# Kernel tuning notes

Hardware: AMD Instinct MI355X
Metric: run time of the kernel (lower is better)

The kernel has to match this reference:

```python
import jax, jax.numpy as jnp
import numpy as np

H = 128  # hidden_size

def _band_agg(h):
    # Equivalent to bmm(adj, h) with adj = degree-normalized tridiagonal
    # (self + left + right neighbor), degree=3 interior, 2 at endpoints,
    # normalization adj/(deg+1e-8) as in the torch module.
    B, S, D = h.shape
    hp = jnp.pad(h, ((0, 0), (1, 1), (0, 0)))
    s = hp[:, :-2] + hp[:, 1:-1] + hp[:, 2:]            # [B,S,D] neighbor sum
    deg = jnp.full((S,), 3.0, dtype=h.dtype).at[0].set(2.0).at[S - 1].set(2.0)
    return s / (deg + 1e-8)[None, :, None]


def setup_inputs() -> dict:
    key = jax.random.key(0)
    ks = jax.random.split(key, 16)
    f32 = jnp.float32
    p = lambda k, shp: (jax.random.normal(k, shp, dtype=f32) * 0.05)
    return {
        "x": jax.random.normal(ks[0], (32, 2048, 6), dtype=f32),
        "enc_w1": p(ks[1], (6, H)),   "enc_b1": p(ks[2], (H,)),
        "enc_w2": p(ks[3], (H, H)),   "enc_b2": p(ks[4], (H,)),
        "gc1_w": p(ks[5], (H, H)),    "gc1_b": p(ks[6], (H,)),
        "gc2_w": p(ks[7], (H, H)),    "gc2_b": p(ks[8], (H,)),
        "gc3_w": p(ks[9], (H, H)),    "gc3_b": p(ks[10], (H,)),
        "cls_w1": p(ks[11], (H, H // 2)), "cls_b1": p(ks[12], (H // 2,)),
        "cls_w2": p(ks[13], (H // 2, 3)), "cls_b2": p(ks[14], (3,)),
    }


def reference(x, enc_w1, enc_b1, enc_w2, enc_b2,
              gc1_w, gc1_b, gc2_w, gc2_b, gc3_w, gc3_b,
              cls_w1, cls_b1, cls_w2, cls_b2):
    # node encoder: Linear -> ReLU -> Linear
    h = jax.nn.relu(x @ enc_w1 + enc_b1) @ enc_w2 + enc_b2
    # three graph convolutions: linear, normalized tridiagonal aggregate, relu
    h = jax.nn.relu(_band_agg(h @ gc1_w + gc1_b))
    h = jax.nn.relu(_band_agg(h @ gc2_w + gc2_b))
    h = jax.nn.relu(_band_agg(h @ gc3_w + gc3_b))
    # AdaptiveAvgPool1d(1) over seq dim after transpose == mean over nodes
    pooled = h.mean(axis=1)                              # [B, H]
    # classifier (dropout inactive in eval)
    return jax.nn.relu(pooled @ cls_w1 + cls_b1) @ cls_w2 + cls_b2
```

## Files before the change

kernel.cpp:

```cpp
#include <hip/hip_runtime.h>

#define SEQ  2048
#define HID  128
#define NB   32
#define TILE 58
#define GX   36
#define MSTR 67

typedef float f2    __attribute__((ext_vector_type(2)));
typedef float f32x4 __attribute__((ext_vector_type(4)));
typedef short bf16x8 __attribute__((ext_vector_type(8)));

__device__ __forceinline__ void split_bf16(float v, short& h, short& l) {
  unsigned u = __float_as_uint(v);
  unsigned r = (u + 0x7fffu + ((u >> 16) & 1u)) >> 16;
  h = (short)r;
  const float hf = __uint_as_float(r << 16);
  const float lo = v - hf;
  unsigned u2 = __float_as_uint(lo);
  unsigned r2 = (u2 + 0x7fffu + ((u2 >> 16) & 1u)) >> 16;
  l = (short)r2;
}

__global__ __launch_bounds__(256) void prep_fold(
    const float* __restrict__ enc_w2, const float* __restrict__ enc_b2,
    const float* __restrict__ gc1_w, const float* __restrict__ gc1_b,
    float* __restrict__ Wp, float* __restrict__ bp)
{
  const int tid = threadIdx.x;
  if (blockIdx.x < 16) {
    const int r = blockIdx.x * 8 + (tid >> 5);
    const int c = (tid & 31) * 4;
    float4 a = make_float4(0.f, 0.f, 0.f, 0.f);
    for (int k = 0; k < 128; ++k) {
      const float w = enc_w2[r * 128 + k];
      const float4 g = *(const float4*)&gc1_w[k * 128 + c];
      a.x = fmaf(w, g.x, a.x); a.y = fmaf(w, g.y, a.y);
      a.z = fmaf(w, g.z, a.z); a.w = fmaf(w, g.w, a.w);
    }
    *(float4*)&Wp[r * 128 + c] = a;
  } else if (tid < 128) {
    float s = gc1_b[tid];
    for (int k = 0; k < 128; ++k) s = fmaf(enc_b2[k], gc1_w[k * 128 + tid], s);
    bp[tid] = s;
  }
}

__global__ __launch_bounds__(256) void prep_shuffle(
    const float* __restrict__ Wp, const float* __restrict__ gc2_w,
    const float* __restrict__ gc3_w, short* __restrict__ Wf)
{
  const int L = blockIdx.y;
  const float* SW = (L == 0) ? Wp : (L == 1) ? gc2_w : gc3_w;
  const int ks = blockIdx.x >> 3, nt = blockIdx.x & 7;
  short* hi = Wf + L * 32768;
  short* lo = hi + 16384;
  for (int f = threadIdx.x; f < 512; f += 256) {
    const int l = f >> 3, j = f & 7;
    const int k = ks * 32 + (l >> 4) * 8 + j;
    const int n = nt * 16 + (l & 15);
    short h, lw;
    split_bf16(SW[k * 128 + n], h, lw);
    const int d = ((ks * 8 + nt) * 64 + l) * 8 + j;
    hi[d] = h; lo[d] = lw;
  }
}

__global__ __launch_bounds__(256) void fused_kernel(
    const float* __restrict__ x,
    const float* __restrict__ enc_w1, const float* __restrict__ enc_b1,
    const short* __restrict__ Wf, const float* __restrict__ bp,
    const float* __restrict__ gc2_b, const float* __restrict__ gc3_b,
    float* __restrict__ partial)
{
  __shared__ float hT[HID * MSTR];
  __shared__ float wsmall[7 * HID];
  __shared__ float psum[256];

  const int tid  = threadIdx.x;
  const int lane = tid & 63;
  const int w    = tid >> 6;
  const int gxb  = blockIdx.x, b = blockIdx.y;
  const int s0   = gxb * TILE;

  for (int f = tid; f < 7 * HID; f += 256)
    wsmall[f] = (f < 6 * HID) ? enc_w1[f] : enc_b1[f - 6 * HID];

  const int sm = s0 - 3 + lane;
  float xv[6];
  if (sm >= 0 && sm < SEQ) {
    const f2* xp = (const f2*)(x + ((long long)b * SEQ + sm) * 6);
    const f2 a0 = xp[0], a1 = xp[1], a2 = xp[2];
    xv[0] = a0.x; xv[1] = a0.y; xv[2] = a1.x;
    xv[3] = a1.y; xv[4] = a2.x; xv[5] = a2.y;
  } else {
    #pragma unroll
    for (int k = 0; k < 6; ++k) xv[k] = 0.f;
  }
  __syncthreads();
  {
    const int c0 = w * 32;
    float4 a4[8];
    #pragma unroll
    for (int q = 0; q < 8; ++q) a4[q] = make_float4(0.f, 0.f, 0.f, 0.f);
    #pragma unroll
    for (int k = 0; k < 6; ++k) {
      #pragma unroll
      for (int q = 0; q < 8; ++q) {
        const float4 wv = *(const float4*)&wsmall[k * HID + c0 + q * 4];
        a4[q].x = fmaf(xv[k], wv.x, a4[q].x);
        a4[q].y = fmaf(xv[k], wv.y, a4[q].y);
        a4[q].z = fmaf(xv[k], wv.z, a4[q].z);
        a4[q].w = fmaf(xv[k], wv.w, a4[q].w);
      }
    }
    #pragma unroll
    for (int q = 0; q < 8; ++q) {
      const float4 bb = *(const float4*)&wsmall[6 * HID + c0 + q * 4];
      const int c = c0 + q * 4;
      hT[(c + 0) * MSTR + lane] = fmaxf(a4[q].x + bb.x, 0.f);
      hT[(c + 1) * MSTR + lane] = fmaxf(a4[q].y + bb.y, 0.f);
      hT[(c + 2) * MSTR + lane] = fmaxf(a4[q].z + bb.z, 0.f);
      hT[(c + 3) * MSTR + lane] = fmaxf(a4[q].w + bb.w, 0.f);
    }
  }
  __syncthreads();

  const int mt   = w * 16 + (lane & 15);
  const int koct = (lane >> 4) * 8;
  const int stt  = s0 - 3 + mt;
  const float invdA = (stt == 0 || stt == SEQ - 1) ? (1.0f / (2.0f + 1e-8f))
                                                   : (1.0f / (3.0f + 1e-8f));
  const int mm = (mt == 0) ? 0 : mt - 1;
  const int mp = (mt == 63) ? 63 : mt + 1;

  #pragma unroll 1
  for (int L = 0; L < 3; ++L) {
    const short* WfL = Wf + L * 32768;
    const bf16x8* Bhi = (const bf16x8*)WfL;
    const bf16x8* Blo = (const bf16x8*)(WfL + 16384);
    const float* bias = (L == 0) ? bp : (L == 1) ? gc2_b : gc3_b;

    f32x4 acc[8];
    #pragma unroll
    for (int nt = 0; nt < 8; ++nt) acc[nt] = (f32x4){0.f, 0.f, 0.f, 0.f};

    #pragma unroll 1
    for (int ks = 0; ks < 4; ++ks) {
      const int fb = ks * 512 + lane;
      bf16x8 bh[8], bl[8];
      #pragma unroll
      for (int nt = 0; nt < 8; ++nt) {
        bh[nt] = Bhi[fb + nt * 64];
        bl[nt] = Blo[fb + nt * 64];
      }
      bf16x8 ah, al;
      const float* pa = &hT[(ks * 32 + koct) * MSTR];
      #pragma unroll
      for (int j = 0; j < 8; ++j) {
        float v;
        if (L == 0) {
          v = pa[j * MSTR + mt];
        } else {
          v = (pa[j * MSTR + mm] + pa[j * MSTR + mt] + pa[j * MSTR + mp]) * invdA;
          v = fmaxf(v, 0.f);
        }
        short h, lo;
        split_bf16(v, h, lo);
        ah[j] = h; al[j] = lo;
      }
      #pragma unroll
      for (int nt = 0; nt < 8; ++nt) {
        acc[nt] = __builtin_amdgcn_mfma_f32_16x16x32_bf16(ah, bh[nt], acc[nt], 0, 0, 0);
        acc[nt] = __builtin_amdgcn_mfma_f32_16x16x32_bf16(ah, bl[nt], acc[nt], 0, 0, 0);
        acc[nt] = __builtin_amdgcn_mfma_f32_16x16x32_bf16(al, bh[nt], acc[nt], 0, 0, 0);
      }
    }
    __syncthreads();

    {
      const int n0 = lane & 15;
      const int mrow0 = w * 16 + (lane >> 4) * 4;
      #pragma unroll
      for (int nt = 0; nt < 8; ++nt) {
        const float bn = bias[nt * 16 + n0];
        float* pw = &hT[(nt * 16 + n0) * MSTR];
        #pragma unroll
        for (int r = 0; r < 4; ++r) {
          const int m = mrow0 + r;
          const int s = s0 - 3 + m;
          const bool vld = (s >= 0 && s < SEQ);
          pw[m] = vld ? (acc[nt][r] + bn) : 0.f;
        }
      }
    }
    __syncthreads();
  }

  {
    const int c = tid & 127, half = tid >> 7;
    float ps = 0.f;
    const float* pc = &hT[c * MSTR];
    #pragma unroll 1
    for (int r = 0; r < 29; ++r) {
      const int m = 3 + half * 29 + r;
      const int s = s0 + half * 29 + r;
      if (s < SEQ) {
        const float invd = (s == 0 || s == SEQ - 1) ? (1.0f / (2.0f + 1e-8f))
                                                    : (1.0f / (3.0f + 1e-8f));
        ps += fmaxf((pc[m - 1] + pc[m] + pc[m + 1]) * invd, 0.f);
      }
    }
    psum[tid] = ps;
  }
  __syncthreads();
  if (tid < 128)
    partial[((long long)b * GX + gxb) * HID + tid] = psum[tid] + psum[tid + 128];
}

__global__ __launch_bounds__(128) void cls_kernel(
    const float* __restrict__ partial,
    const float* __restrict__ w1, const float* __restrict__ b1,
    const float* __restrict__ w2, const float* __restrict__ b2,
    float* __restrict__ out)
{
  __shared__ float ms[128];
  __shared__ float hid[64];
  const int b = blockIdx.x, tid = threadIdx.x;
  float a = 0.f;
  #pragma unroll 1
  for (int g = 0; g < GX; ++g) a += partial[((long long)b * GX + g) * HID + tid];
  ms[tid] = a * (1.0f / 2048.0f);
  __syncthreads();
  if (tid < 64) {
    float h = b1[tid];
    for (int k = 0; k < 128; ++k) h = fmaf(ms[k], w1[k * 64 + tid], h);
    hid[tid] = fmaxf(h, 0.f);
  }
  __syncthreads();
  if (tid < 3) {
    float o = b2[tid];
    for (int k = 0; k < 64; ++k) o = fmaf(hid[k], w2[k * 3 + tid], o);
    out[b * 3 + tid] = o;
  }
}

extern "C" void kernel_launch(void* const* d_in, const int* in_sizes, int n_in,
                              void* d_out, int out_size, void* d_ws, size_t ws_size,
                              hipStream_t stream) {
  (void)in_sizes; (void)n_in; (void)out_size; (void)ws_size;
  const float* x      = (const float*)d_in[0];
  const float* enc_w1 = (const float*)d_in[1];
  const float* enc_b1 = (const float*)d_in[2];
  const float* enc_w2 = (const float*)d_in[3];
  const float* enc_b2 = (const float*)d_in[4];
  const float* gc1_w  = (const float*)d_in[5];
  const float* gc1_b  = (const float*)d_in[6];
  const float* gc2_w  = (const float*)d_in[7];
  const float* gc2_b  = (const float*)d_in[8];
  const float* gc3_w  = (const float*)d_in[9];
  const float* gc3_b  = (const float*)d_in[10];
  const float* cls_w1 = (const float*)d_in[11];
  const float* cls_b1 = (const float*)d_in[12];
  const float* cls_w2 = (const float*)d_in[13];
  const float* cls_b2 = (const float*)d_in[14];

  float* Wp      = (float*)d_ws;
  float* bpv     = Wp + 16384;
  short* Wfrag   = (short*)(bpv + 128);
  float* partial = (float*)(Wfrag + 3 * 2 * 16384);

  prep_fold<<<dim3(17), 256, 0, stream>>>(enc_w2, enc_b2, gc1_w, gc1_b, Wp, bpv);
  prep_shuffle<<<dim3(32, 3), 256, 0, stream>>>(Wp, gc2_w, gc3_w, Wfrag);
  fused_kernel<<<dim3(GX, NB), 256, 0, stream>>>(
      x, enc_w1, enc_b1, Wfrag, bpv, gc2_b, gc3_b, partial);
  cls_kernel<<<dim3(NB), 128, 0, stream>>>(partial, cls_w1, cls_b1, cls_w2, cls_b2,
                                           (float*)d_out);
}
```

Before: 147.4 us.

## Merge weight-fold and bf16 shuffle prep into one kernel; parallelize classifier

The two preprocessing kernels (folding enc_w2 into gc1_w, then splitting and shuffling all three weight matrices into bf16 hi/lo fragments) become a single kernel launch. Each block stages a 32-row k-slice in shared memory before splitting it. This drops one launch and the fp32 Wp round trip through global memory. The classifier kernel now runs 256 threads and splits the partial-sum reduction and the first linear layer across thread groups to shorten the serial loops. The cost is a small 12-block prep grid, which leaves fold parallelism low.

```diff
diff --git a/kernel.cpp b/kernel.cpp
--- a/kernel.cpp
+++ b/kernel.cpp
@@ -22,47 +22,67 @@
   l = (short)r2;
 }
 
-__global__ __launch_bounds__(256) void prep_fold(
+__global__ __launch_bounds__(256) void prep_kernel(
     const float* __restrict__ enc_w2, const float* __restrict__ enc_b2,
     const float* __restrict__ gc1_w, const float* __restrict__ gc1_b,
-    float* __restrict__ Wp, float* __restrict__ bp)
+    const float* __restrict__ gc2_w, const float* __restrict__ gc3_w,
+    short* __restrict__ Wf, float* __restrict__ bp)
 {
+  __shared__ float Wls[32][130];
+  __shared__ float ew2s[32][128];
+  __shared__ float bsum[2][128];
+
+  const int ks = blockIdx.x;
+  const int L  = blockIdx.y;
   const int tid = threadIdx.x;
-  if (blockIdx.x < 16) {
-    const int r = blockIdx.x * 8 + (tid >> 5);
-    const int c = (tid & 31) * 4;
-    float4 a = make_float4(0.f, 0.f, 0.f, 0.f);
-    for (int k = 0; k < 128; ++k) {
-      const float w = enc_w2[r * 128 + k];
-      const float4 g = *(const float4*)&gc1_w[k * 128 + c];
-      a.x = fmaf(w, g.x, a.x); a.y = fmaf(w, g.y, a.y);
-      a.z = fmaf(w, g.z, a.z); a.w = fmaf(w, g.w, a.w);
-    }
-    *(float4*)&Wp[r * 128 + c] = a;
-  } else if (tid < 128) {
-    float s = gc1_b[tid];
-    for (int k = 0; k < 128; ++k) s = fmaf(enc_b2[k], gc1_w[k * 128 + tid], s);
-    bp[tid] = s;
-  }
-}
-
-__global__ __launch_bounds__(256) void prep_shuffle(
-    const float* __restrict__ Wp, const float* __restrict__ gc2_w,
-    const float* __restrict__ gc3_w, short* __restrict__ Wf)
-{
-  const int L = blockIdx.y;
-  const float* SW = (L == 0) ? Wp : (L == 1) ? gc2_w : gc3_w;
-  const int ks = blockIdx.x >> 3, nt = blockIdx.x & 7;
-  short* hi = Wf + L * 32768;
+
+  if (L == 0) {
+    for (int f = tid; f < 32 * 128; f += 256)
+      ew2s[f >> 7][f & 127] = enc_w2[(ks * 32 + (f >> 7)) * 128 + (f & 127)];
+    __syncthreads();
+    {
+      const int c = tid & 127, rh = tid >> 7;
+      float acc[16];
+      #pragma unroll
+      for (int i = 0; i < 16; ++i) acc[i] = 0.f;
+      #pragma unroll 4
+      for (int k = 0; k < 128; ++k) {
+        const float g = gc1_w[k * 128 + c];
+        #pragma unroll
+        for (int i = 0; i < 16; ++i)
+          acc[i] = fmaf(ew2s[rh * 16 + i][k], g, acc[i]);
+      }
+      #pragma unroll
+      for (int i = 0; i < 16; ++i) Wls[rh * 16 + i][c] = acc[i];
+    }
+    if (ks == 0) {
+      const int c = tid & 127, kh = tid >> 7;
+      float s = 0.f;
+      #pragma unroll 4
+      for (int k0 = 0; k0 < 64; ++k0) {
+        const int k = kh * 64 + k0;
+        s = fmaf(enc_b2[k], gc1_w[k * 128 + c], s);
+      }
+      bsum[kh][c] = s;
+    }
+    __syncthreads();
+    if (ks == 0 && tid < 128) bp[tid] = gc1_b[tid] + bsum[0][tid] + bsum[1][tid];
+  } else {
+    const float* SW = (L == 1) ? gc2_w : gc3_w;
+    for (int f = tid; f < 32 * 128; f += 256)
+      Wls[f >> 7][f & 127] = SW[(ks * 32 + (f >> 7)) * 128 + (f & 127)];
+    __syncthreads();
+  }
+
+  short* hi = Wf + L * 32768 + ks * 4096;
   short* lo = hi + 16384;
-  for (int f = threadIdx.x; f < 512; f += 256) {
-    const int l = f >> 3, j = f & 7;
-    const int k = ks * 32 + (l >> 4) * 8 + j;
-    const int n = nt * 16 + (l & 15);
+  for (int f = tid; f < 4096; f += 256) {
+    const int nt = f >> 9, l = (f >> 3) & 63, j = f & 7;
+    const int kk = (l >> 4) * 8 + j;
+    const int n  = nt * 16 + (l & 15);
     short h, lw;
-    split_bf16(SW[k * 128 + n], h, lw);
-    const int d = ((ks * 8 + nt) * 64 + l) * 8 + j;
-    hi[d] = h; lo[d] = lw;
+    split_bf16(Wls[kk][n], h, lw);
+    hi[f] = h; lo[f] = lw;
   }
 }
 
@@ -218,28 +238,48 @@
     partial[((long long)b * GX + gxb) * HID + tid] = psum[tid] + psum[tid + 128];
 }
 
-__global__ __launch_bounds__(128) void cls_kernel(
+__global__ __launch_bounds__(256) void cls_kernel(
     const float* __restrict__ partial,
     const float* __restrict__ w1, const float* __restrict__ b1,
     const float* __restrict__ w2, const float* __restrict__ b2,
     float* __restrict__ out)
 {
+  __shared__ float red[256];
   __shared__ float ms[128];
+  __shared__ float hp[4][64];
   __shared__ float hid[64];
   const int b = blockIdx.x, tid = threadIdx.x;
-  float a = 0.f;
-  #pragma unroll 1
-  for (int g = 0; g < GX; ++g) a += partial[((long long)b * GX + g) * HID + tid];
-  ms[tid] = a * (1.0f / 2048.0f);
-  __syncthreads();
-  if (tid < 64) {
-    float h = b1[tid];
-    for (int k = 0; k < 128; ++k) h = fmaf(ms[k], w1[k * 64 + tid], h);
-    hid[tid] = fmaxf(h, 0.f);
-  }
-  __syncthreads();
+
+  {
+    const int c = tid & 127, gh = tid >> 7;
+    float a = 0.f;
+    #pragma unroll 2
+    for (int g = gh; g < GX; g += 2)
+      a += partial[((long long)b * GX + g) * HID + c];
+    red[tid] = a;
+  }
+  __syncthreads();
+  if (tid < 128) ms[tid] = (red[tid] + red[tid + 128]) * (1.0f / 2048.0f);
+  __syncthreads();
+
+  {
+    const int c = tid & 63, kq = tid >> 6;
+    float h = 0.f;
+    #pragma unroll 8
+    for (int k0 = 0; k0 < 32; ++k0) {
+      const int k = kq * 32 + k0;
+      h = fmaf(ms[k], w1[k * 64 + c], h);
+    }
+    hp[kq][c] = h;
+  }
+  __syncthreads();
+  if (tid < 64)
+    hid[tid] = fmaxf(hp[0][tid] + hp[1][tid] + hp[2][tid] + hp[3][tid] + b1[tid], 0.f);
+  __syncthreads();
+
   if (tid < 3) {
     float o = b2[tid];
+    #pragma unroll 8
     for (int k = 0; k < 64; ++k) o = fmaf(hid[k], w2[k * 3 + tid], o);
     out[b * 3 + tid] = o;
   }
@@ -265,15 +305,14 @@
   const float* cls_w2 = (const float*)d_in[13];
   const float* cls_b2 = (const float*)d_in[14];
 
-  float* Wp      = (float*)d_ws;
-  float* bpv     = Wp + 16384;
-  short* Wfrag   = (short*)(bpv + 128);
-  float* partial = (float*)(Wfrag + 3 * 2 * 16384);
-
-  prep_fold<<<dim3(17), 256, 0, stream>>>(enc_w2, enc_b2, gc1_w, gc1_b, Wp, bpv);
-  prep_shuffle<<<dim3(32, 3), 256, 0, stream>>>(Wp, gc2_w, gc3_w, Wfrag);
+  short* Wfrag   = (short*)d_ws;
+  float* bpv     = (float*)(Wfrag + 3 * 2 * 16384);
+  float* partial = bpv + 128;
+
+  prep_kernel<<<dim3(4, 3), 256, 0, stream>>>(
+      enc_w2, enc_b2, gc1_w, gc1_b, gc2_w, gc3_w, Wfrag, bpv);
   fused_kernel<<<dim3(GX, NB), 256, 0, stream>>>(
       x, enc_w1, enc_b1, Wfrag, bpv, gc2_b, gc3_b, partial);
-  cls_kernel<<<dim3(NB), 128, 0, stream>>>(partial, cls_w1, cls_b1, cls_w2, cls_b2,
+  cls_kernel<<<dim3(NB), 256, 0, stream>>>(partial, cls_w1, cls_b1, cls_w2, cls_b2,
                                            (float*)d_out);
 }
```

Result: slower. 151.4 us (+2.7%).
